# Kernel optimization log

Hardware: AMD Instinct MI355X
Metric: run time of the kernel (lower is better)

## Reference

```python
import jax, jax.numpy as jnp
import numpy as np

NUM_WIRES = 18
NUM_LAYERS = 3
BATCH = 64
DIM = 2 ** NUM_WIRES


def _apply_ry(psi, theta, w):
    # RY(t) = [[cos(t/2), -sin(t/2)], [sin(t/2), cos(t/2)]] on wire w (wire 0 = MSB)
    B = psi.shape[0]
    c = jnp.cos(theta * 0.5).astype(psi.dtype)
    s = jnp.sin(theta * 0.5).astype(psi.dtype)
    p = psi.reshape(B, 2 ** w, 2, -1)
    a, b = p[:, :, 0], p[:, :, 1]
    return jnp.stack([c * a - s * b, s * a + c * b], axis=2).reshape(B, -1)


def _apply_rz(psi, theta, w):
    # RZ(t) = diag(e^{-i t/2}, e^{+i t/2}) on wire w
    B = psi.shape[0]
    half = (theta * 0.5).astype(jnp.complex64)
    p0 = jnp.exp(-1j * half)
    p1 = jnp.exp(1j * half)
    p = psi.reshape(B, 2 ** w, 2, -1)
    return jnp.stack([p0 * p[:, :, 0], p1 * p[:, :, 1]], axis=2).reshape(B, -1)


def _apply_cnot_adjacent(psi, w):
    # CNOT with control w, target w+1: flip target bit where control bit = 1
    B = psi.shape[0]
    p = psi.reshape(B, 2 ** w, 2, 2, -1)
    p = p.at[:, :, 1].set(p[:, :, 1, ::-1])
    return p.reshape(B, -1)


def _expval_z(psi, w):
    # <Z_w> = P(bit_w = 0) - P(bit_w = 1)
    B = psi.shape[0]
    prob = (psi.real ** 2 + psi.imag ** 2).reshape(B, 2 ** w, 2, -1)
    p = prob.sum(axis=(1, 3))  # (B, 2)
    return p[:, 0] - p[:, 1]


def _circuit(psi, params):
    for layer in range(params.shape[0]):
        for w in range(NUM_WIRES):
            psi = _apply_ry(psi, params[layer, 0, w], w)
            psi = _apply_rz(psi, params[layer, 1, w], w)
        for w in range(NUM_WIRES - 1):
            psi = _apply_cnot_adjacent(psi, w)
    # expvals of PauliZ on every wire -> (B, num_wires)
    return jnp.stack([_expval_z(psi, w) for w in range(NUM_WIRES)], axis=-1)


def setup_inputs() -> dict:
    key = jax.random.key(0)
    k1, k2, k3, k4, k5 = jax.random.split(key, 5)
    state_re = jax.random.normal(k1, (BATCH, DIM), dtype=jnp.float32)
    state_im = jax.random.normal(k2, (BATCH, DIM), dtype=jnp.float32)
    norm = jnp.sqrt(jnp.sum(state_re ** 2 + state_im ** 2, axis=-1, keepdims=True))
    state_re = state_re / norm
    state_im = state_im / norm
    params = jax.random.normal(k3, (NUM_LAYERS, 2, NUM_WIRES), dtype=jnp.float32)
    head_w = jax.random.normal(k4, (1, NUM_WIRES), dtype=jnp.float32) / np.sqrt(NUM_WIRES)
    head_b = jax.random.normal(k5, (1,), dtype=jnp.float32) / np.sqrt(NUM_WIRES)
    return {"state_re": state_re, "state_im": state_im, "params": params,
            "head_w": head_w, "head_b": head_b}


def reference(state_re, state_im, params, head_w, head_b):
    psi = (state_re + 1j * state_im).astype(jnp.complex64)  # (B, 2^n)
    feats = _circuit(psi, params)                            # (B, n)
    out = feats @ head_w.T + head_b                          # (B, 1)
    return out[:, 0]
```

## Files before the change

kernel.cpp:

```cpp
#include <hip/hip_runtime.h>


#define LROW 36u
#define LDSW 2304u

typedef float f32x2 __attribute__((ext_vector_type(2)));

static __device__ __forceinline__ float rfl(float x) {
    return __int_as_float(__builtin_amdgcn_readfirstlane(__float_as_int(x)));
}

static __device__ __forceinline__ f32x2 unpk(unsigned u) {
    f32x2 v;
    v.x = __uint_as_float(u << 16);
    v.y = __uint_as_float(u & 0xFFFF0000u);
    return v;
}

static __device__ __forceinline__ unsigned packbf(f32x2 a) {
    unsigned ua = __float_as_uint(a.x); ua += 0x7FFFu + ((ua >> 16) & 1u);
    unsigned ub = __float_as_uint(a.y); ub += 0x7FFFu + ((ub >> 16) & 1u);
    return (ua >> 16) | (ub & 0xFFFF0000u);
}

static __device__ __forceinline__ void sq_pair2(f32x2& a0, f32x2& a1,
                                                f32x2 ry, f32x2 pz) {
    f32x2 m, n, t1, p;
    asm("v_pk_mul_f32 %0, %1, %2 op_sel:[1,0] op_sel_hi:[1,1]"
        : "=v"(m) : "s"(ry), "v"(a1));
    asm("v_pk_mul_f32 %0, %1, %2 op_sel:[0,0] op_sel_hi:[0,1]"
        : "=v"(n) : "s"(ry), "v"(a1));
    asm("v_pk_fma_f32 %0, %1, %2, %3 op_sel:[1,0,0] op_sel_hi:[1,1,1]"
        : "=v"(t1) : "s"(ry), "v"(a0), "v"(n));
    asm("v_pk_fma_f32 %0, %1, %0, %2 op_sel:[0,0,0] op_sel_hi:[0,1,1] neg_lo:[0,0,1] neg_hi:[0,0,1]"
        : "+v"(a0) : "s"(ry), "v"(m));
    asm("v_pk_mul_f32 %0, %1, %2 op_sel:[1,1] op_sel_hi:[1,0]"
        : "=v"(p) : "s"(pz), "v"(t1));
    asm("v_pk_fma_f32 %0, %1, %2, %3 op_sel:[0,0,0] op_sel_hi:[0,1,1] neg_lo:[0,0,1] neg_hi:[0,0,0]"
        : "=v"(a1) : "s"(pz), "v"(t1), "v"(p));
}

template<int J>
__device__ __forceinline__ void sqg2(f32x2* a, f32x2 ry, f32x2 pz) {
#pragma unroll
    for (int r = 0; r < 32; ++r) {
        if (((r >> J) & 1) == 0) {
            sq_pair2(a[r], a[r + (1 << J)], ry, pz);
        }
    }
}

static __device__ __forceinline__ void t1_float(f32x2* a, float* Lb, int l, unsigned tb) {
#pragma unroll
    for (int g = 0; g < 8; ++g)
#pragma unroll
        for (int c = 0; c < 4; ++c)
            Lb[tb + g * 288 + c * 36] = a[4*g+c].x;
#pragma unroll
    for (int q = 0; q < 8; ++q) {
        const float4 v = *(const float4*)&Lb[(unsigned)l * LROW + (q << 2)];
        a[4*q+0].x = v.x; a[4*q+1].x = v.y; a[4*q+2].x = v.z; a[4*q+3].x = v.w;
    }
#pragma unroll
    for (int g = 0; g < 8; ++g)
#pragma unroll
        for (int c = 0; c < 4; ++c)
            Lb[tb + g * 288 + c * 36] = a[4*g+c].y;
#pragma unroll
    for (int q = 0; q < 8; ++q) {
        const float4 v = *(const float4*)&Lb[(unsigned)l * LROW + (q << 2)];
        a[4*q+0].y = v.x; a[4*q+1].y = v.y; a[4*q+2].y = v.z; a[4*q+3].y = v.w;
    }
}

static __device__ __forceinline__ void pack_t2(f32x2* a, float* Lb, int l, unsigned tb,
                                               unsigned v[8][4]) {
    unsigned* Lu = (unsigned*)Lb;
#pragma unroll
    for (int q = 0; q < 8; ++q) {
        uint4 pv;
        pv.x = packbf(a[4*q+0]); pv.y = packbf(a[4*q+1]);
        pv.z = packbf(a[4*q+2]); pv.w = packbf(a[4*q+3]);
        *(uint4*)&Lu[(unsigned)l * LROW + (q << 2)] = pv;
    }
#pragma unroll
    for (int g = 0; g < 8; ++g)
#pragma unroll
        for (int c = 0; c < 4; ++c)
            v[g][c] = Lu[tb + g * 288 + c * 36];
}

struct BCoef2 { f32x2 RY[7], PZ[7]; };

static __device__ __forceinline__ void passB_coefs(BCoef2& k, const float* pl) {
#pragma unroll
    for (int j = 0; j < 7; ++j) {
        const int w = 6 - j;
        float sv, cv;
        __sincosf(0.5f * pl[w], &sv, &cv);
        k.RY[j].x = rfl(cv); k.RY[j].y = rfl(sv);
        __sincosf(pl[18 + w], &sv, &cv);
        k.PZ[j].x = rfl(cv); k.PZ[j].y = rfl(sv);
    }
}

static __device__ __forceinline__ void passB_body(f32x2* a, float* Lb,
                                                  const BCoef2& k, int l) {
    const unsigned tb = (unsigned)(l & 1) * 144u + (unsigned)(l >> 1);
    sqg2<4>(a, k.RY[4], k.PZ[4]);
    sqg2<3>(a, k.RY[3], k.PZ[3]);
    sqg2<2>(a, k.RY[2], k.PZ[2]);
    t1_float(a, Lb, l, tb);
    sqg2<4>(a, k.RY[6], k.PZ[6]);
    sqg2<3>(a, k.RY[5], k.PZ[5]);
    sqg2<2>(a, k.RY[1], k.PZ[1]);
    sqg2<1>(a, k.RY[0], k.PZ[0]);
}

__global__ __launch_bounds__(128) void passB1_k(const float* re, const float* im,
                                                unsigned* u, const float* __restrict__ params)
{
    __shared__ float lds[2 * LDSW];
    const int t   = threadIdx.x;
    const int l   = t & 63;
    const int wib = t >> 6;
    float* Lb = lds + wib * LDSW;
    const int wv  = ((int)blockIdx.x << 1) | wib;
    const int b   = wv >> 7;
    const int mid = wv & 127;
    const int L5 = (l >> 5) & 1, L4 = (l >> 4) & 1, L3 = (l >> 3) & 1, L2 = (l >> 2) & 1;
    const int L1 = (l >> 1) & 1, L0 = l & 1;

    const unsigned base = ((unsigned)b << 18) | ((unsigned)mid << 4);
    const unsigned sel  = (L5 << 17) | (L4 << 16) | (L3 << 12) | (L2 << 11) | (L1 << 3) | (L0 << 2);

    f32x2 a[32];
#pragma unroll
    for (int g = 0; g < 8; ++g) {
        const unsigned n = base + sel + ((unsigned)g << 13);
        const float4 vr = *(const float4*)&re[n];
        const float4 vi = *(const float4*)&im[n];
        a[4*g+0].x = vr.x; a[4*g+0].y = vi.x;
        a[4*g+1].x = vr.y; a[4*g+1].y = vi.y;
        a[4*g+2].x = vr.z; a[4*g+2].y = vi.z;
        a[4*g+3].x = vr.w; a[4*g+3].y = vi.w;
    }

    BCoef2 k; passB_coefs(k, params);
    passB_body(a, Lb, k, l);

    unsigned v[8][4];
    pack_t2(a, Lb, l, (unsigned)L0 * 144u + (unsigned)(l >> 1), v);

#pragma unroll
    for (int g = 0; g < 8; ++g) {
        const int h = (L5 << 6) | (L4 << 5) | (g << 2) | (L3 << 1) | L2;
        const unsigned n = base + ((unsigned)h << 11) + (L1 << 3) + (L0 << 2);
        *(uint4*)&u[n] = make_uint4(v[g][0], v[g][1], v[g][2], v[g][3]);
    }
}

__global__ __launch_bounds__(128) void passBk_k(const unsigned* __restrict__ src,
                                                unsigned* __restrict__ dst,
                                                const float* __restrict__ params, int layer)
{
    __shared__ float lds[2 * LDSW];
    const int t   = threadIdx.x;
    const int l   = t & 63;
    const int wib = t >> 6;
    float* Lb = lds + wib * LDSW;
    const int wv  = ((int)blockIdx.x << 1) | wib;
    const int b   = wv >> 7;
    const int mid = wv & 127;
    const int L5 = (l >> 5) & 1, L4 = (l >> 4) & 1, L3 = (l >> 3) & 1, L2 = (l >> 2) & 1;
    const int L1 = (l >> 1) & 1, L0 = l & 1;

    const unsigned base = ((unsigned)b << 18) | ((unsigned)mid << 4);
    const unsigned sel  = (L5 << 17) | (L4 << 16) | (L3 << 12) | (L2 << 11) | (L1 << 3) | (L0 << 2);

    f32x2 a[32];
#pragma unroll
    for (int g = 0; g < 8; ++g) {
        const unsigned n = base + sel + ((unsigned)g << 13);
        const uint4 pv = *(const uint4*)&src[n];
        a[4*g+0] = unpk(pv.x);
        a[4*g+1] = unpk(pv.y);
        a[4*g+2] = unpk(pv.z);
        a[4*g+3] = unpk(pv.w);
    }

    BCoef2 k; passB_coefs(k, params + layer * 36);
    passB_body(a, Lb, k, l);

    unsigned v[8][4];
    pack_t2(a, Lb, l, (unsigned)L0 * 144u + (unsigned)(l >> 1), v);

#pragma unroll
    for (int g = 0; g < 8; ++g) {
        int h = (L5 << 6) | (L4 << 5) | (g << 2) | (L3 << 1) | L2;
        int x = h ^ (h >> 1); x ^= x >> 2; x ^= x >> 4;
        const unsigned n = base + ((unsigned)x << 11) + (L1 << 3) + (L0 << 2);
        *(uint4*)&dst[n] = make_uint4(v[g][0], v[g][1], v[g][2], v[g][3]);
    }
}

template<bool FIRST, bool FINAL>
__global__ __launch_bounds__(128) void passA_k(const unsigned* __restrict__ src,
                                               unsigned* __restrict__ dst,
                                               const float* __restrict__ params, int layer,
                                               const float* __restrict__ hw,
                                               const float* __restrict__ hb,
                                               float* __restrict__ out)
{
    __shared__ float lds[2 * LDSW];
    const int t   = threadIdx.x;
    const int l   = t & 63;
    const int wib = t >> 6;
    float* Lb = lds + wib * LDSW;
    const int wv  = ((int)blockIdx.x << 1) | wib;
    const int b   = wv >> 7;
    const int L   = wv & 127;
    const int hip = FIRST ? (L ^ (L >> 1)) : L;
    const int n11 = L & 1;
    const unsigned baseL = ((unsigned)b << 18) | ((unsigned)hip << 11);
    const unsigned baseS = ((unsigned)b << 18) | ((unsigned)L << 11);

    uint4 U[8];
#pragma unroll
    for (int g = 0; g < 8; ++g)
        U[g] = *(const uint4*)&src[baseL + ((unsigned)g << 8) + ((unsigned)l << 2)];

    f32x2 RY2[11], PZ2[11];
    const float* pl = params + layer * 36;
#pragma unroll
    for (int p = 0; p < 11; ++p) {
        const int w = 17 - p;
        float sv, cv;
        __sincosf(0.5f * pl[w], &sv, &cv);
        RY2[p].x = rfl(cv); RY2[p].y = rfl(sv);
        __sincosf(pl[18 + w], &sv, &cv);
        PZ2[p].x = rfl(cv); PZ2[p].y = rfl(sv);
    }

    f32x2 a[32];
#pragma unroll
    for (int g = 0; g < 8; ++g) {
        a[4*g+0] = unpk(U[g].x);
        a[4*g+1] = unpk(U[g].y);
        a[4*g+2] = unpk(U[g].z);
        a[4*g+3] = unpk(U[g].w);
        sq_pair2(a[4*g+0], a[4*g+2], RY2[1], PZ2[1]);
        sq_pair2(a[4*g+1], a[4*g+3], RY2[1], PZ2[1]);
        sq_pair2(a[4*g+0], a[4*g+1], RY2[0], PZ2[0]);
        sq_pair2(a[4*g+2], a[4*g+3], RY2[0], PZ2[0]);
    }

    sqg2<4>(a, RY2[10], PZ2[10]);
    sqg2<3>(a, RY2[9],  PZ2[9]);
    sqg2<2>(a, RY2[8],  PZ2[8]);

    {
        const int side   = (l >> 5) & 1;
        const float c7   = RY2[7].x;
        const float bco  = side ? RY2[7].y : -RY2[7].y;
        const float qc   = side ? PZ2[7].x : 1.f;
        const float qs   = side ? PZ2[7].y : 0.f;
#pragma unroll
        for (int r = 0; r < 32; ++r) {
            const float pr = __shfl_xor(a[r].x, 32);
            const float pi = __shfl_xor(a[r].y, 32);
            const float tr = fmaf(c7, a[r].x, bco * pr);
            const float ti = fmaf(c7, a[r].y, bco * pi);
            a[r].x = fmaf(qc, tr, -(qs * ti));
            a[r].y = fmaf(qc, ti,  (qs * tr));
        }
    }

    const unsigned tb = (unsigned)((l >> 5) & 1) * 144u + (unsigned)(l & 31);
    t1_float(a, Lb, l, tb);

    sqg2<4>(a, RY2[6], PZ2[6]);
    sqg2<3>(a, RY2[5], PZ2[5]);
    sqg2<2>(a, RY2[4], PZ2[4]);
    sqg2<1>(a, RY2[3], PZ2[3]);
    sqg2<0>(a, RY2[2], PZ2[2]);

    const int msk = n11 ? 0x1FF : 0;

    if (!FINAL) {
        unsigned v[8][4];
        pack_t2(a, Lb, l, tb, v);
#pragma unroll
        for (int g = 0; g < 8; ++g) {
            int h = (g << 6) | l;
            int x = h ^ (h >> 1); x ^= x >> 2; x ^= x >> 4; x ^= x >> 8;
            x ^= msk;
            const int y = x & 1;
            uint4 pv;
            pv.x = y ? v[g][2] : v[g][0];
            pv.y = y ? v[g][3] : v[g][1];
            pv.z = y ? v[g][1] : v[g][3];
            pv.w = y ? v[g][0] : v[g][2];
            *(uint4*)&dst[baseS + ((unsigned)x << 2)] = pv;
        }
    } else {
#pragma unroll
        for (int q = 0; q < 8; ++q)
            *(float4*)&Lb[(unsigned)l * LROW + (q << 2)] =
                make_float4(a[4*q+0].x, a[4*q+1].x, a[4*q+2].x, a[4*q+3].x);
#pragma unroll
        for (int g = 0; g < 8; ++g)
#pragma unroll
            for (int c = 0; c < 4; ++c)
                a[4*g+c].x = Lb[tb + g * 288 + c * 36];
#pragma unroll
        for (int q = 0; q < 8; ++q)
            *(float4*)&Lb[(unsigned)l * LROW + (q << 2)] =
                make_float4(a[4*q+0].y, a[4*q+1].y, a[4*q+2].y, a[4*q+3].y);
#pragma unroll
        for (int g = 0; g < 8; ++g)
#pragma unroll
            for (int c = 0; c < 4; ++c)
                a[4*g+c].y = Lb[tb + g * 288 + c * 36];

        float Ghi = 0.f;
#pragma unroll
        for (int j = 0; j < 7; ++j) {
            const float wv_ = hw[6 - j];
            Ghi += ((L >> j) & 1) ? -wv_ : wv_;
        }
        float acc = 0.f;
#pragma unroll
        for (int g = 0; g < 8; ++g) {
            int h = (g << 6) | l;
            int x = h ^ (h >> 1); x ^= x >> 2; x ^= x >> 4; x ^= x >> 8;
            x ^= msk;
            const float q0 = fmaf(a[4*g+0].x, a[4*g+0].x, a[4*g+0].y * a[4*g+0].y);
            const float q1 = fmaf(a[4*g+1].x, a[4*g+1].x, a[4*g+1].y * a[4*g+1].y);
            const float q2 = fmaf(a[4*g+2].x, a[4*g+2].x, a[4*g+2].y * a[4*g+2].y);
            const float q3 = fmaf(a[4*g+3].x, a[4*g+3].x, a[4*g+3].y * a[4*g+3].y);
            const float psum = (q0 + q1) + (q2 + q3);
            const float d1   = (q0 + q1) - (q2 + q3);
            const float d0   = (q0 - q1) - (q2 - q3);
            float Gm = 0.f;
#pragma unroll
            for (int j = 0; j < 9; ++j) {
                const float wv_ = hw[15 - j];
                Gm += ((x >> j) & 1) ? -wv_ : wv_;
            }
            const float ys = (x & 1) ? -1.f : 1.f;
            acc += psum * (Ghi + Gm) + ys * fmaf(d1, hw[16], d0 * hw[17]);
        }
        if (L == 0 && l == 0) acc += hb[0];
#pragma unroll
        for (int off = 32; off > 0; off >>= 1) acc += __shfl_xor(acc, off);
        if (l == 0) atomicAdd(&out[b], acc);
    }
}

extern "C" void kernel_launch(void* const* d_in, const int* in_sizes, int n_in,
                              void* d_out, int out_size, void* d_ws, size_t ws_size,
                              hipStream_t stream)
{
    const float* re0    = (const float*)d_in[0];
    const float* im0    = (const float*)d_in[1];
    unsigned* u0        = (unsigned*)d_in[0];
    unsigned* u1        = (unsigned*)d_in[1];
    const float* params = (const float*)d_in[2];
    const float* hw     = (const float*)d_in[3];
    const float* hb     = (const float*)d_in[4];
    float* out          = (float*)d_out;
    (void)in_sizes; (void)n_in; (void)d_ws; (void)ws_size;

    hipMemsetAsync(out, 0, (size_t)out_size * sizeof(float), stream);

    const dim3 grid(4096), blk(128);
    passB1_k             <<<grid, blk, 0, stream>>>(re0, im0, u0, params);
    passA_k<true,  false><<<grid, blk, 0, stream>>>(u0, u1, params, 0, nullptr, nullptr, nullptr);
    passBk_k             <<<grid, blk, 0, stream>>>(u1, u0, params, 1);
    passA_k<false, false><<<grid, blk, 0, stream>>>(u0, u1, params, 1, nullptr, nullptr, nullptr);
    passBk_k             <<<grid, blk, 0, stream>>>(u1, u0, params, 2);
    passA_k<false, true ><<<grid, blk, 0, stream>>>(u0, nullptr, params, 2, hw, hb, out);
}
```

Before: 372.6 us.

## Swizzle LDS transpose layout, use permlane32 swap, add occupancy hints

Replaces the padded LDS row stride of 36 floats with an unpadded 32-float row and an XOR swizzle on the column index. This shrinks the LDS footprint while still avoiding bank conflicts in the transpose. The cross-half exchange in passA now uses permlane32_swap instead of shuffle-xor through LDS, and the inline-asm packed complex rotation is rewritten with vector builtins for the compiler to schedule. All kernels also get a min-blocks-per-CU launch bound of 5, which may constrain registers and risk spills.

```diff
diff --git a/kernel.cpp b/kernel.cpp
--- a/kernel.cpp
+++ b/kernel.cpp
@@ -1,10 +1,15 @@
 #include <hip/hip_runtime.h>
 
 
-#define LROW 36u
-#define LDSW 2304u
+#define LROW 32u
+#define LDSW 2048u
 
 typedef float f32x2 __attribute__((ext_vector_type(2)));
+typedef unsigned u32x2 __attribute__((ext_vector_type(2)));
+
+static __device__ __forceinline__ unsigned lA(unsigned row, unsigned col) {
+    return row * LROW + (((col & 28u) ^ ((row & 7u) << 2)) | (col & 3u));
+}
 
 static __device__ __forceinline__ float rfl(float x) {
     return __int_as_float(__builtin_amdgcn_readfirstlane(__float_as_int(x)));
@@ -25,19 +30,17 @@
 
 static __device__ __forceinline__ void sq_pair2(f32x2& a0, f32x2& a1,
                                                 f32x2 ry, f32x2 pz) {
-    f32x2 m, n, t1, p;
-    asm("v_pk_mul_f32 %0, %1, %2 op_sel:[1,0] op_sel_hi:[1,1]"
-        : "=v"(m) : "s"(ry), "v"(a1));
-    asm("v_pk_mul_f32 %0, %1, %2 op_sel:[0,0] op_sel_hi:[0,1]"
-        : "=v"(n) : "s"(ry), "v"(a1));
-    asm("v_pk_fma_f32 %0, %1, %2, %3 op_sel:[1,0,0] op_sel_hi:[1,1,1]"
-        : "=v"(t1) : "s"(ry), "v"(a0), "v"(n));
-    asm("v_pk_fma_f32 %0, %1, %0, %2 op_sel:[0,0,0] op_sel_hi:[0,1,1] neg_lo:[0,0,1] neg_hi:[0,0,1]"
-        : "+v"(a0) : "s"(ry), "v"(m));
-    asm("v_pk_mul_f32 %0, %1, %2 op_sel:[1,1] op_sel_hi:[1,0]"
-        : "=v"(p) : "s"(pz), "v"(t1));
-    asm("v_pk_fma_f32 %0, %1, %2, %3 op_sel:[0,0,0] op_sel_hi:[0,1,1] neg_lo:[0,0,1] neg_hi:[0,0,0]"
-        : "=v"(a1) : "s"(pz), "v"(t1), "v"(p));
+    const f32x2 cc = __builtin_shufflevector(ry, ry, 0, 0);
+    const f32x2 ss = __builtin_shufflevector(ry, ry, 1, 1);
+    const f32x2 m  = ss * a1;
+    const f32x2 t1 = __builtin_elementwise_fma(ss, a0, cc * a1);
+    a0 = __builtin_elementwise_fma(cc, a0, -m);
+    const f32x2 pcv = __builtin_shufflevector(pz, pz, 0, 0);
+    const f32x2 psv = __builtin_shufflevector(pz, pz, 1, 1);
+    f32x2 swn;
+    swn.x = -t1.y;
+    swn.y =  t1.x;
+    a1 = __builtin_elementwise_fma(pcv, t1, psv * swn);
 }
 
 template<int J>
@@ -50,30 +53,32 @@
     }
 }
 
-static __device__ __forceinline__ void t1_float(f32x2* a, float* Lb, int l, unsigned tb) {
+static __device__ __forceinline__ void t1_float(f32x2* a, float* Lb, int l,
+                                                unsigned rbase, unsigned pos) {
 #pragma unroll
     for (int g = 0; g < 8; ++g)
 #pragma unroll
         for (int c = 0; c < 4; ++c)
-            Lb[tb + g * 288 + c * 36] = a[4*g+c].x;
+            Lb[lA(g * 8 + rbase + c, pos)] = a[4*g+c].x;
 #pragma unroll
     for (int q = 0; q < 8; ++q) {
-        const float4 v = *(const float4*)&Lb[(unsigned)l * LROW + (q << 2)];
+        const float4 v = *(const float4*)&Lb[lA((unsigned)l, q << 2)];
         a[4*q+0].x = v.x; a[4*q+1].x = v.y; a[4*q+2].x = v.z; a[4*q+3].x = v.w;
     }
 #pragma unroll
     for (int g = 0; g < 8; ++g)
 #pragma unroll
         for (int c = 0; c < 4; ++c)
-            Lb[tb + g * 288 + c * 36] = a[4*g+c].y;
+            Lb[lA(g * 8 + rbase + c, pos)] = a[4*g+c].y;
 #pragma unroll
     for (int q = 0; q < 8; ++q) {
-        const float4 v = *(const float4*)&Lb[(unsigned)l * LROW + (q << 2)];
+        const float4 v = *(const float4*)&Lb[lA((unsigned)l, q << 2)];
         a[4*q+0].y = v.x; a[4*q+1].y = v.y; a[4*q+2].y = v.z; a[4*q+3].y = v.w;
     }
 }
 
-static __device__ __forceinline__ void pack_t2(f32x2* a, float* Lb, int l, unsigned tb,
+static __device__ __forceinline__ void pack_t2(f32x2* a, float* Lb, int l,
+                                               unsigned rbase, unsigned pos,
                                                unsigned v[8][4]) {
     unsigned* Lu = (unsigned*)Lb;
 #pragma unroll
@@ -81,13 +86,13 @@
         uint4 pv;
         pv.x = packbf(a[4*q+0]); pv.y = packbf(a[4*q+1]);
         pv.z = packbf(a[4*q+2]); pv.w = packbf(a[4*q+3]);
-        *(uint4*)&Lu[(unsigned)l * LROW + (q << 2)] = pv;
+        *(uint4*)&Lu[lA((unsigned)l, q << 2)] = pv;
     }
 #pragma unroll
     for (int g = 0; g < 8; ++g)
 #pragma unroll
         for (int c = 0; c < 4; ++c)
-            v[g][c] = Lu[tb + g * 288 + c * 36];
+            v[g][c] = Lu[lA(g * 8 + rbase + c, pos)];
 }
 
 struct BCoef2 { f32x2 RY[7], PZ[7]; };
@@ -106,19 +111,20 @@
 
 static __device__ __forceinline__ void passB_body(f32x2* a, float* Lb,
                                                   const BCoef2& k, int l) {
-    const unsigned tb = (unsigned)(l & 1) * 144u + (unsigned)(l >> 1);
+    const unsigned rbase = (unsigned)(l & 1) * 4u;
+    const unsigned pos   = (unsigned)(l >> 1);
     sqg2<4>(a, k.RY[4], k.PZ[4]);
     sqg2<3>(a, k.RY[3], k.PZ[3]);
     sqg2<2>(a, k.RY[2], k.PZ[2]);
-    t1_float(a, Lb, l, tb);
+    t1_float(a, Lb, l, rbase, pos);
     sqg2<4>(a, k.RY[6], k.PZ[6]);
     sqg2<3>(a, k.RY[5], k.PZ[5]);
     sqg2<2>(a, k.RY[1], k.PZ[1]);
     sqg2<1>(a, k.RY[0], k.PZ[0]);
 }
 
-__global__ __launch_bounds__(128) void passB1_k(const float* re, const float* im,
-                                                unsigned* u, const float* __restrict__ params)
+__global__ __launch_bounds__(128, 5) void passB1_k(const float* re, const float* im,
+                                                   unsigned* u, const float* __restrict__ params)
 {
     __shared__ float lds[2 * LDSW];
     const int t   = threadIdx.x;
@@ -150,7 +156,7 @@
     passB_body(a, Lb, k, l);
 
     unsigned v[8][4];
-    pack_t2(a, Lb, l, (unsigned)L0 * 144u + (unsigned)(l >> 1), v);
+    pack_t2(a, Lb, l, (unsigned)L0 * 4u, (unsigned)(l >> 1), v);
 
 #pragma unroll
     for (int g = 0; g < 8; ++g) {
@@ -160,9 +166,9 @@
     }
 }
 
-__global__ __launch_bounds__(128) void passBk_k(const unsigned* __restrict__ src,
-                                                unsigned* __restrict__ dst,
-                                                const float* __restrict__ params, int layer)
+__global__ __launch_bounds__(128, 5) void passBk_k(const unsigned* __restrict__ src,
+                                                   unsigned* __restrict__ dst,
+                                                   const float* __restrict__ params, int layer)
 {
     __shared__ float lds[2 * LDSW];
     const int t   = threadIdx.x;
@@ -193,7 +199,7 @@
     passB_body(a, Lb, k, l);
 
     unsigned v[8][4];
-    pack_t2(a, Lb, l, (unsigned)L0 * 144u + (unsigned)(l >> 1), v);
+    pack_t2(a, Lb, l, (unsigned)L0 * 4u, (unsigned)(l >> 1), v);
 
 #pragma unroll
     for (int g = 0; g < 8; ++g) {
@@ -205,12 +211,12 @@
 }
 
 template<bool FIRST, bool FINAL>
-__global__ __launch_bounds__(128) void passA_k(const unsigned* __restrict__ src,
-                                               unsigned* __restrict__ dst,
-                                               const float* __restrict__ params, int layer,
-                                               const float* __restrict__ hw,
-                                               const float* __restrict__ hb,
-                                               float* __restrict__ out)
+__global__ __launch_bounds__(128, 5) void passA_k(const unsigned* __restrict__ src,
+                                                  unsigned* __restrict__ dst,
+                                                  const float* __restrict__ params, int layer,
+                                                  const float* __restrict__ hw,
+                                                  const float* __restrict__ hb,
+                                                  float* __restrict__ out)
 {
     __shared__ float lds[2 * LDSW];
     const int t   = threadIdx.x;
@@ -260,24 +266,30 @@
     sqg2<2>(a, RY2[8],  PZ2[8]);
 
     {
-        const int side   = (l >> 5) & 1;
-        const float c7   = RY2[7].x;
-        const float bco  = side ? RY2[7].y : -RY2[7].y;
-        const float qc   = side ? PZ2[7].x : 1.f;
-        const float qs   = side ? PZ2[7].y : 0.f;
+        const int side = (l >> 5) & 1;
+        const float c7 = RY2[7].x, s7 = RY2[7].y;
+        const float cA = side ? s7 : c7;
+        const float cB = side ? c7 : -s7;
+        const float qc = side ? PZ2[7].x : 1.f;
+        const float qs = side ? PZ2[7].y : 0.f;
 #pragma unroll
         for (int r = 0; r < 32; ++r) {
-            const float pr = __shfl_xor(a[r].x, 32);
-            const float pi = __shfl_xor(a[r].y, 32);
-            const float tr = fmaf(c7, a[r].x, bco * pr);
-            const float ti = fmaf(c7, a[r].y, bco * pi);
+            const u32x2 rx = __builtin_amdgcn_permlane32_swap(
+                __float_as_uint(a[r].x), __float_as_uint(a[r].x), false, false);
+            const u32x2 ry = __builtin_amdgcn_permlane32_swap(
+                __float_as_uint(a[r].y), __float_as_uint(a[r].y), false, false);
+            const float lox = __uint_as_float(rx.x), hix = __uint_as_float(rx.y);
+            const float loy = __uint_as_float(ry.x), hiy = __uint_as_float(ry.y);
+            const float tr = fmaf(cA, lox, cB * hix);
+            const float ti = fmaf(cA, loy, cB * hiy);
             a[r].x = fmaf(qc, tr, -(qs * ti));
             a[r].y = fmaf(qc, ti,  (qs * tr));
         }
     }
 
-    const unsigned tb = (unsigned)((l >> 5) & 1) * 144u + (unsigned)(l & 31);
-    t1_float(a, Lb, l, tb);
+    const unsigned rbase = (unsigned)((l >> 5) & 1) * 4u;
+    const unsigned pos   = (unsigned)(l & 31);
+    t1_float(a, Lb, l, rbase, pos);
 
     sqg2<4>(a, RY2[6], PZ2[6]);
     sqg2<3>(a, RY2[5], PZ2[5]);
@@ -289,7 +301,7 @@
 
     if (!FINAL) {
         unsigned v[8][4];
-        pack_t2(a, Lb, l, tb, v);
+        pack_t2(a, Lb, l, rbase, pos, v);
 #pragma unroll
         for (int g = 0; g < 8; ++g) {
             int h = (g << 6) | l;
@@ -306,22 +318,22 @@
     } else {
 #pragma unroll
         for (int q = 0; q < 8; ++q)
-            *(float4*)&Lb[(unsigned)l * LROW + (q << 2)] =
+            *(float4*)&Lb[lA((unsigned)l, q << 2)] =
                 make_float4(a[4*q+0].x, a[4*q+1].x, a[4*q+2].x, a[4*q+3].x);
 #pragma unroll
         for (int g = 0; g < 8; ++g)
 #pragma unroll
             for (int c = 0; c < 4; ++c)
-                a[4*g+c].x = Lb[tb + g * 288 + c * 36];
+                a[4*g+c].x = Lb[lA(g * 8 + rbase + c, pos)];
 #pragma unroll
         for (int q = 0; q < 8; ++q)
-            *(float4*)&Lb[(unsigned)l * LROW + (q << 2)] =
+            *(float4*)&Lb[lA((unsigned)l, q << 2)] =
                 make_float4(a[4*q+0].y, a[4*q+1].y, a[4*q+2].y, a[4*q+3].y);
 #pragma unroll
         for (int g = 0; g < 8; ++g)
 #pragma unroll
             for (int c = 0; c < 4; ++c)
-                a[4*g+c].y = Lb[tb + g * 288 + c * 36];
+                a[4*g+c].y = Lb[lA(g * 8 + rbase + c, pos)];
 
         float Ghi = 0.f;
 #pragma unroll
```

Measured after the change: 514.9 us. 38.2% more time.
